# Kernel tuning notes

Measured on AMD Instinct MI355X. Metric: run time of the kernel, lower is better.

Reference implementation:

```python
import math
import jax, jax.numpy as jnp
import numpy as np

D_MODEL = 1024
NUM_HEADS = 16
MAX_SEQ_LEN = 2048
THETA = 10000.0


def setup_inputs() -> dict:
    key = jax.random.key(0)
    ks = jax.random.split(key, 5)
    B, S, D = 2, 2048, D_MODEL
    std = math.sqrt(2.0 / (D + D))
    x = jax.random.normal(ks[0], (B, S, D), dtype=jnp.float32)
    wq = jax.random.normal(ks[1], (D, D), dtype=jnp.float32) * std
    wk = jax.random.normal(ks[2], (D, D), dtype=jnp.float32) * std
    wv = jax.random.normal(ks[3], (D, D), dtype=jnp.float32) * std
    wo = jax.random.normal(ks[4], (D, D), dtype=jnp.float32) * std
    return {"x": x, "wq": wq, "wk": wk, "wv": wv, "wo": wo}


def _rope_tables(seq_len: int, d_k: int):
    # angles[i, k] = i / theta^(2k/d_k), k over d_k//2 pairs
    inv_freq = 1.0 / (THETA ** (jnp.arange(0, d_k, 2, dtype=jnp.float32) / d_k))
    angles = jnp.arange(seq_len, dtype=jnp.float32)[:, None] * inv_freq[None, :]  # [S, d_k/2]
    return jnp.cos(angles), jnp.sin(angles)


def _apply_rope(x, cos, sin):
    # x: [..., S, d_k]; cos/sin: [S, d_k/2], broadcast over leading dims
    x_even = x[..., ::2]
    x_odd = x[..., 1::2]
    r_even = x_even * cos - x_odd * sin
    r_odd = x_even * sin + x_odd * cos
    return jnp.stack([r_even, r_odd], axis=-1).reshape(x.shape)


def reference(x, wq, wk, wv, wo):
    B, S, D = x.shape
    H = NUM_HEADS
    dk = D // H

    def split_heads(t):  # [B,S,D] -> [B,H,S,dk]
        return t.reshape(B, S, H, dk).transpose(0, 2, 1, 3)

    Q = split_heads(x @ wq.T)
    K = split_heads(x @ wk.T)
    V = split_heads(x @ wv.T)

    cos, sin = _rope_tables(S, dk)
    Q = _apply_rope(Q, cos, sin)
    K = _apply_rope(K, cos, sin)

    scores = jnp.einsum('bhqd,bhkd->bhqk', Q, K) / jnp.sqrt(jnp.float32(dk))
    mask = jnp.tril(jnp.ones((S, S), dtype=bool))  # causal: q can attend k <= q
    neg_inf = jnp.float32(-jnp.inf)
    scores = jnp.where(mask, scores, neg_inf)
    m = jnp.max(scores, axis=-1, keepdims=True)
    m = jnp.where(jnp.isinf(m), jnp.zeros_like(m), m)
    exp_scores = jnp.exp(scores - m)
    exp_scores = jnp.where(mask, exp_scores, 0.0)
    attn = exp_scores / (jnp.sum(exp_scores, axis=-1, keepdims=True) + 1e-9)
    out = jnp.einsum('bhqk,bhkd->bhqd', attn, V)  # [B,H,S,dk]
    out = out.transpose(0, 2, 1, 3).reshape(B, S, D)
    return out @ wo.T
```

## Files before the change

kernel.cpp:

```cpp
#include <hip/hip_runtime.h>
#include <stdint.h>

typedef unsigned short u16;
typedef unsigned int u32;
typedef __bf16 bf16x8 __attribute__((ext_vector_type(8)));
typedef float f32x4 __attribute__((ext_vector_type(4)));
typedef unsigned short u16x8 __attribute__((ext_vector_type(8)));

#define D_MODEL 1024
#define SEQ 2048
#define NH 16
#define DK 64
#define NROWS 4096

static __device__ __forceinline__ u16 f2bf(float f) {
  u32 u = __float_as_uint(f);
  u = (u + 0x7FFFu + ((u >> 16) & 1u)) >> 16;
  return (u16)u;
}
static __device__ __forceinline__ float bf2f(u16 h) {
  return __uint_as_float(((u32)h) << 16);
}
static __device__ __forceinline__ f32x4 mfma16(bf16x8 a, bf16x8 b, f32x4 c) {
  return __builtin_amdgcn_mfma_f32_16x16x32_bf16(a, b, c, 0, 0, 0);
}
static __device__ __forceinline__ void gload16(const void* g, void* l) {
  __builtin_amdgcn_global_load_lds(
      (const __attribute__((address_space(1))) void*)g,
      (__attribute__((address_space(3))) void*)l, 16, 0, 0);
}

__global__ __launch_bounds__(256) void k_cast(
    const float* __restrict__ x, const float* __restrict__ wq,
    const float* __restrict__ wk, const float* __restrict__ wv,
    const float* __restrict__ wo, u16* __restrict__ xb, u16* __restrict__ wqb,
    u16* __restrict__ wkb, u16* __restrict__ wvb, u16* __restrict__ wob) {
  size_t e = ((size_t)blockIdx.x * 256 + threadIdx.x) * 8;
  const float* s;
  u16* d;
  size_t off;
  if (e < (size_t)NROWS * D_MODEL) {
    s = x; d = xb; off = e;
  } else {
    size_t r = e - (size_t)NROWS * D_MODEL;
    unsigned wi = (unsigned)(r >> 20);
    off = r & 1048575u;
    s = wi == 0 ? wq : wi == 1 ? wk : wi == 2 ? wv : wo;
    d = wi == 0 ? wqb : wi == 1 ? wkb : wi == 2 ? wvb : wob;
  }
  float4 a = *(const float4*)(s + off);
  float4 b = *(const float4*)(s + off + 4);
  u16x8 o;
  o[0] = f2bf(a.x); o[1] = f2bf(a.y); o[2] = f2bf(a.z); o[3] = f2bf(a.w);
  o[4] = f2bf(b.x); o[5] = f2bf(b.y); o[6] = f2bf(b.z); o[7] = f2bf(b.w);
  *(u16x8*)(d + off) = o;
}

__global__ __launch_bounds__(256) void k_tab(float* __restrict__ ct, float* __restrict__ st) {
  int i = blockIdx.x * 256 + threadIdx.x;
  int s = i >> 5, p = i & 31;
  double ang = (double)s * pow(10000.0, -(double)p / 32.0);
  ct[i] = (float)cos(ang);
  st[i] = (float)sin(ang);
}

template <bool MULTI, bool OUTF32>
__global__ __launch_bounds__(256, 1) void k_gemm(
    const u16* __restrict__ A, const u16* __restrict__ B0,
    const u16* __restrict__ B1, const u16* __restrict__ B2,
    u16* __restrict__ Cb, float* __restrict__ Cf, int ldc) {
  constexpr int K = 1024;
  const int mb = blockIdx.x, nb = blockIdx.y;
  const int tid = threadIdx.x;
  const int lane = tid & 63, w = tid >> 6;
  const int lq = lane & 15, lg = lane >> 4;
  const int wm = w >> 1, wn = w & 1;
  __shared__ __align__(16) u16 As[128 * 32];
  __shared__ __align__(16) u16 Bs[128 * 32];

  const u16* Bp;
  if (MULTI) {
    int sel = nb >> 3;
    Bp = sel == 0 ? B0 : (sel == 1 ? B1 : B2);
  } else {
    Bp = B0;
  }
  int nloc = MULTI ? (nb & 7) * 128 : nb * 128;
  const char* Ab = (const char*)A + (size_t)mb * 128 * 2048;
  const char* Bb = (const char*)Bp + (size_t)nloc * 2048;

  const int srow = tid >> 2;
  const int scb = (tid & 3) * 16;

  f32x4 zero4 = {0.f, 0.f, 0.f, 0.f};
  f32x4 acc[4][4];
#pragma unroll
  for (int i = 0; i < 4; ++i)
#pragma unroll
    for (int j = 0; j < 4; ++j) acc[i][j] = zero4;

  for (int k0 = 0; k0 < K; k0 += 32) {
#pragma unroll
    for (int c = 0; c < 2; ++c) {
      int o = c * 4096 + tid * 16;
      const char* ga = Ab + (size_t)(c * 64 + srow) * 2048 + k0 * 2 + scb;
      const char* gb = Bb + (size_t)(c * 64 + srow) * 2048 + k0 * 2 + scb;
      gload16(ga, (char*)As + o);
      gload16(gb, (char*)Bs + o);
    }
    __syncthreads();
    bf16x8 af[4], bfr[4];
#pragma unroll
    for (int i = 0; i < 4; ++i) {
      af[i] = *(const bf16x8*)((const char*)As + (wm * 64 + i * 16 + lq) * 64 + lg * 16);
      bfr[i] = *(const bf16x8*)((const char*)Bs + (wn * 64 + i * 16 + lq) * 64 + lg * 16);
    }
#pragma unroll
    for (int i = 0; i < 4; ++i)
#pragma unroll
      for (int j = 0; j < 4; ++j) acc[i][j] = mfma16(af[i], bfr[j], acc[i][j]);
    __syncthreads();
  }

#pragma unroll
  for (int i = 0; i < 4; ++i) {
#pragma unroll
    for (int r = 0; r < 4; ++r) {
      size_t rowg = (size_t)(mb * 128 + wm * 64 + i * 16 + lg * 4 + r);
#pragma unroll
      for (int j = 0; j < 4; ++j) {
        int colg = nb * 128 + wn * 64 + j * 16 + lq;
        if (OUTF32)
          Cf[rowg * ldc + colg] = acc[i][j][r];
        else
          Cb[rowg * ldc + colg] = f2bf(acc[i][j][r]);
      }
    }
  }
}

__global__ __launch_bounds__(256) void k_rope(const u16* __restrict__ qkv,
                                              const float* __restrict__ ct,
                                              const float* __restrict__ st,
                                              u16* __restrict__ qh, u16* __restrict__ kh) {
  int gi = blockIdx.x * 256 + threadIdx.x;
  int row = gi >> 7;
  int col = (gi & 127) << 3;
  int h = col >> 6, d0 = col & 63;
  int b = row >> 11, s = row & 2047;
  const int srcoff = blockIdx.y ? 1024 : 0;
  u16x8 v = *(const u16x8*)(qkv + (size_t)row * 3072 + srcoff + col);
  const float* cp = ct + s * 32 + (d0 >> 1);
  const float* sp = st + s * 32 + (d0 >> 1);
  u16x8 o;
#pragma unroll
  for (int i = 0; i < 4; ++i) {
    float ev = bf2f(v[2 * i]), od = bf2f(v[2 * i + 1]);
    float c = cp[i], sn = sp[i];
    o[2 * i] = f2bf(ev * c - od * sn);
    o[2 * i + 1] = f2bf(ev * sn + od * c);
  }
  u16* dst = blockIdx.y ? kh : qh;
  *(u16x8*)(dst + (((size_t)(b * 16 + h) * SEQ + s) << 6) + d0) = o;
}

__global__ __launch_bounds__(256) void k_vtrans(const u16* __restrict__ qkv,
                                                u16* __restrict__ vt) {
  __shared__ __align__(16) u16 t[64][72];
  int sb = blockIdx.x, bh = blockIdx.y;
  int b = bh >> 4, h = bh & 15;
  int tid = threadIdx.x;
#pragma unroll
  for (int c = 0; c < 2; ++c) {
    int o = tid * 8 + c * 2048;
    int r = o >> 6, d = o & 63;
    u16x8 v = *(const u16x8*)(qkv + (size_t)(b * SEQ + sb * 64 + r) * 3072 + 2048 + h * 64 + d);
    *(u16x8*)&t[r][d] = v;
  }
  __syncthreads();
#pragma unroll
  for (int c = 0; c < 2; ++c) {
    int o = tid * 8 + c * 2048;
    int d = o >> 6, si = o & 63;
    u16x8 v;
#pragma unroll
    for (int j = 0; j < 8; ++j) v[j] = t[si + j][d];
    *(u16x8*)(vt + ((size_t)bh * 64 + d) * SEQ + sb * 64 + si) = v;
  }
}

__global__ __launch_bounds__(512, 2) void k_attn(const u16* __restrict__ qh,
                                                 const u16* __restrict__ kh,
                                                 const u16* __restrict__ vt,
                                                 u16* __restrict__ ao) {
  const int xb_ = (int)blockIdx.x;
  const int qb = (xb_ & 1) ? (xb_ >> 1) : (15 - (xb_ >> 1));
  const int bh = blockIdx.y;
  const int tid = threadIdx.x;
  const int w = tid >> 6;
  const int lane = tid & 63;
  const int lq = lane & 15;
  const int lg = lane >> 4;

  __shared__ __align__(16) u16 Kl[64 * 64];
  __shared__ __align__(16) u16 Vl[64 * 64];
  __shared__ __align__(16) u16 Pl[8][16 * 64];

  const int q0 = qb * 128;
  const int qtop = q0 + w * 16;
  const int qrow = qtop + lq;

  const u16* qptr = qh + ((size_t)bh * SEQ + qrow) * DK + lg * 8;
  bf16x8 qf0 = *(const bf16x8*)qptr;
  bf16x8 qf1 = *(const bf16x8*)(qptr + 32);

  f32x4 zero4 = {0.f, 0.f, 0.f, 0.f};
  f32x4 accO[4];
  accO[0] = zero4; accO[1] = zero4; accO[2] = zero4; accO[3] = zero4;
  float m_run = -1e30f, l_run = 0.f;
  const float SCL = 0.180336880f;

  const int nkv = (qb + 1) * 2;
  const int srow = tid >> 3;
  const int scb = (tid & 7) * 16;

  uint4 kreg, vreg;
  kreg = *(const uint4*)((const char*)(kh + ((size_t)bh * SEQ + srow) * DK) + scb);
  vreg = *(const uint4*)((const char*)(vt + ((size_t)bh * DK + srow) * SEQ) + scb);

  for (int t = 0; t < nkv; ++t) {
    {
      int ad = (srow * 128 + scb) ^ ((srow & 7) << 4);
      *(uint4*)((char*)Kl + ad) = kreg;
      *(uint4*)((char*)Vl + ad) = vreg;
    }
    __syncthreads();

    uint4 k2, v2;
    if (t + 1 < nkv) {
      int k0n = (t + 1) * 64;
      k2 = *(const uint4*)((const char*)(kh + ((size_t)bh * SEQ + k0n + srow) * DK) + scb);
      v2 = *(const uint4*)((const char*)(vt + ((size_t)bh * DK + srow) * SEQ + k0n) + scb);
    } else {
      k2 = kreg; v2 = vreg;
    }

    const int k0 = t * 64;
    if (k0 <= qtop + 15) {
      f32x4 sa[4];
      sa[0] = zero4; sa[1] = zero4; sa[2] = zero4; sa[3] = zero4;
      __builtin_amdgcn_s_setprio(1);
#pragma unroll
      for (int kt = 0; kt < 4; ++kt) {
        int krow = kt * 16 + lq;
        int base = krow * 128 + lg * 16;
        int swz = (krow & 7) << 4;
        bf16x8 kf0 = *(const bf16x8*)((const char*)Kl + (base ^ swz));
        bf16x8 kf1 = *(const bf16x8*)((const char*)Kl + ((base + 64) ^ swz));
        sa[kt] = mfma16(kf0, qf0, sa[kt]);
        sa[kt] = mfma16(kf1, qf1, sa[kt]);
      }
      __builtin_amdgcn_s_setprio(0);

      float p[16];
      float pm = -1e30f;
#pragma unroll
      for (int kt = 0; kt < 4; ++kt) {
#pragma unroll
        for (int r = 0; r < 4; ++r) {
          int key = k0 + kt * 16 + lg * 4 + r;
          float sv = sa[kt][r] * SCL;
          sv = (key <= qrow) ? sv : -1e30f;
          p[kt * 4 + r] = sv;
          pm = fmaxf(pm, sv);
        }
      }
      pm = fmaxf(pm, __shfl_xor(pm, 16));
      pm = fmaxf(pm, __shfl_xor(pm, 32));
      const bool resc = __any(pm > m_run + 8.0f);
      float mnew = resc ? fmaxf(m_run, pm) : m_run;
      float rs = 0.f;
#pragma unroll
      for (int i = 0; i < 16; ++i) {
        p[i] = __builtin_amdgcn_exp2f(p[i] - mnew);
        rs += p[i];
      }
      rs += __shfl_xor(rs, 16);
      rs += __shfl_xor(rs, 32);
      if (resc) {
        float alpha = __builtin_amdgcn_exp2f(m_run - mnew);
        l_run = l_run * alpha + rs;
        m_run = mnew;
#pragma unroll
        for (int r = 0; r < 4; ++r) {
          float ar = __shfl(alpha, lg * 4 + r);
#pragma unroll
          for (int dt = 0; dt < 4; ++dt) accO[dt][r] *= ar;
        }
      } else {
        l_run += rs;
      }

      {
        int swz = (lq & 7) << 4;
#pragma unroll
        for (int kt = 0; kt < 4; ++kt) {
          u32 w0, w1;
          asm("v_cvt_pk_bf16_f32 %0, %1, %2"
              : "=v"(w0) : "v"(p[kt * 4 + 0]), "v"(p[kt * 4 + 1]));
          asm("v_cvt_pk_bf16_f32 %0, %1, %2"
              : "=v"(w1) : "v"(p[kt * 4 + 2]), "v"(p[kt * 4 + 3]));
          int a0 = (lq * 128 + (kt * 16 + lg * 4) * 2) ^ swz;
          int a1 = (lq * 128 + (kt * 16 + lg * 4 + 2) * 2) ^ swz;
          *(u32*)((char*)Pl[w] + a0) = w0;
          *(u32*)((char*)Pl[w] + a1) = w1;
        }
      }
      {
        int swz = (lq & 7) << 4;
        bf16x8 pa0 = *(const bf16x8*)((const char*)Pl[w] + ((lq * 128 + lg * 16) ^ swz));
        bf16x8 pa1 = *(const bf16x8*)((const char*)Pl[w] + ((lq * 128 + 64 + lg * 16) ^ swz));
        __builtin_amdgcn_s_setprio(1);
#pragma unroll
        for (int dt = 0; dt < 4; ++dt) {
          int vrow = dt * 16 + lq;
          int vb = vrow * 128 + lg * 16;
          int vs = (vrow & 7) << 4;
          bf16x8 v0 = *(const bf16x8*)((const char*)Vl + (vb ^ vs));
          bf16x8 v1 = *(const bf16x8*)((const char*)Vl + ((vb + 64) ^ vs));
          accO[dt] = mfma16(pa0, v0, accO[dt]);
          accO[dt] = mfma16(pa1, v1, accO[dt]);
        }
        __builtin_amdgcn_s_setprio(0);
      }
    }
    __syncthreads();
    kreg = k2; vreg = v2;
  }

  const int b = bh >> 4, h = bh & 15;
#pragma unroll
  for (int r = 0; r < 4; ++r) {
    float lr = __shfl(l_run, lg * 4 + r);
    float inv = 1.f / (lr + 1e-9f);
    int qq = qtop + lg * 4 + r;
    u16* orow = ao + ((size_t)b * SEQ + qq) * D_MODEL + h * DK;
#pragma unroll
    for (int dt = 0; dt < 4; ++dt) orow[dt * 16 + lq] = f2bf(accO[dt][r] * inv);
  }
}

extern "C" void kernel_launch(void* const* d_in, const int* in_sizes, int n_in,
                              void* d_out, int out_size, void* d_ws, size_t ws_size,
                              hipStream_t stream) {
  const float* x = (const float*)d_in[0];
  const float* wq = (const float*)d_in[1];
  const float* wk = (const float*)d_in[2];
  const float* wv = (const float*)d_in[3];
  const float* wo = (const float*)d_in[4];
  float* out = (float*)d_out;
  char* ws = (char*)d_ws;

  u16* xb   = (u16*)(ws + 0);
  u16* wqb  = (u16*)(ws + 8388608);
  u16* wkb  = (u16*)(ws + 10485760);
  u16* wvb  = (u16*)(ws + 12582912);
  u16* wob  = (u16*)(ws + 14680064);
  u16* qkv  = (u16*)(ws + 16777216);
  u16* qhb  = (u16*)(ws + 41943040);
  u16* khb  = (u16*)(ws + 50331648);
  u16* vtb  = (u16*)(ws + 58720256);
  u16* aob  = (u16*)(ws + 67108864);
  float* ct = (float*)(ws + 75497472);
  float* st = (float*)(ws + 75759616);

  k_cast<<<4096, 256, 0, stream>>>(x, wq, wk, wv, wo, xb, wqb, wkb, wvb, wob);
  k_tab<<<256, 256, 0, stream>>>(ct, st);
  k_gemm<true, false><<<dim3(32, 24), 256, 0, stream>>>(xb, wqb, wkb, wvb, qkv, nullptr, 3072);
  k_rope<<<dim3(2048, 2), 256, 0, stream>>>(qkv, ct, st, qhb, khb);
  k_vtrans<<<dim3(32, 32), 256, 0, stream>>>(qkv, vtb);
  k_attn<<<dim3(16, 32), 512, 0, stream>>>(qhb, khb, vtb, aob);
  k_gemm<false, true><<<dim3(32, 8), 256, 0, stream>>>(aob, wob, nullptr, nullptr, nullptr, out, 1024);
}
```

Baseline: 140.6 us.

## Pair complementary causal query blocks per workgroup with double-buffered direct LDS loads

Each attention workgroup now processes two query blocks (qb and 15-qb) so every block does equal causal work, and both query tiles reuse each K/V tile staged in shared memory. K/V loads go straight to a double-buffered LDS area via an async-style global-to-LDS load, replacing register staging. The grid is halved, so fewer workgroups run concurrently, and LDS use grows with the second buffer.

```diff
diff --git a/kernel.cpp b/kernel.cpp
--- a/kernel.cpp
+++ b/kernel.cpp
@@ -189,12 +189,105 @@
   }
 }
 
+static __device__ __forceinline__ void attn_tile(
+    const u16* Kl, const u16* Vl, u16* Plw, int k0, int qrow, int lq, int lg,
+    bf16x8 qf0, bf16x8 qf1, float& m_run, float& l_run, f32x4* accO) {
+  f32x4 zero4 = {0.f, 0.f, 0.f, 0.f};
+  const float SCL = 0.180336880f;
+  f32x4 sa[4];
+  sa[0] = zero4; sa[1] = zero4; sa[2] = zero4; sa[3] = zero4;
+  __builtin_amdgcn_s_setprio(1);
+#pragma unroll
+  for (int kt = 0; kt < 4; ++kt) {
+    int krow = kt * 16 + lq;
+    int base = krow * 128 + lg * 16;
+    int swz = (krow & 7) << 4;
+    bf16x8 kf0 = *(const bf16x8*)((const char*)Kl + (base ^ swz));
+    bf16x8 kf1 = *(const bf16x8*)((const char*)Kl + ((base + 64) ^ swz));
+    sa[kt] = mfma16(kf0, qf0, sa[kt]);
+    sa[kt] = mfma16(kf1, qf1, sa[kt]);
+  }
+  __builtin_amdgcn_s_setprio(0);
+
+  float p[16];
+  float pm = -1e30f;
+#pragma unroll
+  for (int kt = 0; kt < 4; ++kt) {
+#pragma unroll
+    for (int r = 0; r < 4; ++r) {
+      int key = k0 + kt * 16 + lg * 4 + r;
+      float sv = sa[kt][r] * SCL;
+      sv = (key <= qrow) ? sv : -1e30f;
+      p[kt * 4 + r] = sv;
+      pm = fmaxf(pm, sv);
+    }
+  }
+  pm = fmaxf(pm, __shfl_xor(pm, 16));
+  pm = fmaxf(pm, __shfl_xor(pm, 32));
+  const bool resc = __any(pm > m_run + 8.0f);
+  float mnew = resc ? fmaxf(m_run, pm) : m_run;
+  float rs = 0.f;
+#pragma unroll
+  for (int i = 0; i < 16; ++i) {
+    p[i] = __builtin_amdgcn_exp2f(p[i] - mnew);
+    rs += p[i];
+  }
+  rs += __shfl_xor(rs, 16);
+  rs += __shfl_xor(rs, 32);
+  if (resc) {
+    float alpha = __builtin_amdgcn_exp2f(m_run - mnew);
+    l_run = l_run * alpha + rs;
+    m_run = mnew;
+#pragma unroll
+    for (int r = 0; r < 4; ++r) {
+      float ar = __shfl(alpha, lg * 4 + r);
+#pragma unroll
+      for (int dt = 0; dt < 4; ++dt) accO[dt][r] *= ar;
+    }
+  } else {
+    l_run += rs;
+  }
+
+  {
+    int swz = (lq & 7) << 4;
+#pragma unroll
+    for (int kt = 0; kt < 4; ++kt) {
+      u32 w0, w1;
+      asm("v_cvt_pk_bf16_f32 %0, %1, %2"
+          : "=v"(w0) : "v"(p[kt * 4 + 0]), "v"(p[kt * 4 + 1]));
+      asm("v_cvt_pk_bf16_f32 %0, %1, %2"
+          : "=v"(w1) : "v"(p[kt * 4 + 2]), "v"(p[kt * 4 + 3]));
+      int a0 = (lq * 128 + (kt * 16 + lg * 4) * 2) ^ swz;
+      int a1 = (lq * 128 + (kt * 16 + lg * 4 + 2) * 2) ^ swz;
+      *(u32*)((char*)Plw + a0) = w0;
+      *(u32*)((char*)Plw + a1) = w1;
+    }
+  }
+  {
+    int swz = (lq & 7) << 4;
+    bf16x8 pa0 = *(const bf16x8*)((const char*)Plw + ((lq * 128 + lg * 16) ^ swz));
+    bf16x8 pa1 = *(const bf16x8*)((const char*)Plw + ((lq * 128 + 64 + lg * 16) ^ swz));
+    __builtin_amdgcn_s_setprio(1);
+#pragma unroll
+    for (int dt = 0; dt < 4; ++dt) {
+      int vrow = dt * 16 + lq;
+      int vb = vrow * 128 + lg * 16;
+      int vs = (vrow & 7) << 4;
+      bf16x8 v0 = *(const bf16x8*)((const char*)Vl + (vb ^ vs));
+      bf16x8 v1 = *(const bf16x8*)((const char*)Vl + ((vb + 64) ^ vs));
+      accO[dt] = mfma16(pa0, v0, accO[dt]);
+      accO[dt] = mfma16(pa1, v1, accO[dt]);
+    }
+    __builtin_amdgcn_s_setprio(0);
+  }
+}
+
 __global__ __launch_bounds__(512, 2) void k_attn(const u16* __restrict__ qh,
                                                  const u16* __restrict__ kh,
                                                  const u16* __restrict__ vt,
                                                  u16* __restrict__ ao) {
-  const int xb_ = (int)blockIdx.x;
-  const int qb = (xb_ & 1) ? (xb_ >> 1) : (15 - (xb_ >> 1));
+  const int qb1 = (int)blockIdx.x;
+  const int qb2 = 15 - qb1;
   const int bh = blockIdx.y;
   const int tid = threadIdx.x;
   const int w = tid >> 6;
@@ -202,151 +295,74 @@
   const int lq = lane & 15;
   const int lg = lane >> 4;
 
-  __shared__ __align__(16) u16 Kl[64 * 64];
-  __shared__ __align__(16) u16 Vl[64 * 64];
+  __shared__ __align__(16) u16 Kd[2][64 * 64];
+  __shared__ __align__(16) u16 Vd[2][64 * 64];
   __shared__ __align__(16) u16 Pl[8][16 * 64];
 
-  const int q0 = qb * 128;
-  const int qtop = q0 + w * 16;
-  const int qrow = qtop + lq;
-
-  const u16* qptr = qh + ((size_t)bh * SEQ + qrow) * DK + lg * 8;
-  bf16x8 qf0 = *(const bf16x8*)qptr;
-  bf16x8 qf1 = *(const bf16x8*)(qptr + 32);
+  const int qtop1 = qb1 * 128 + w * 16;
+  const int qtop2 = qb2 * 128 + w * 16;
+  const int qrow1 = qtop1 + lq;
+  const int qrow2 = qtop2 + lq;
+
+  const u16* qp1 = qh + ((size_t)bh * SEQ + qrow1) * DK + lg * 8;
+  const u16* qp2 = qh + ((size_t)bh * SEQ + qrow2) * DK + lg * 8;
+  bf16x8 qa0 = *(const bf16x8*)qp1;
+  bf16x8 qa1 = *(const bf16x8*)(qp1 + 32);
+  bf16x8 qb0 = *(const bf16x8*)qp2;
+  bf16x8 qb1f = *(const bf16x8*)(qp2 + 32);
 
   f32x4 zero4 = {0.f, 0.f, 0.f, 0.f};
-  f32x4 accO[4];
-  accO[0] = zero4; accO[1] = zero4; accO[2] = zero4; accO[3] = zero4;
-  float m_run = -1e30f, l_run = 0.f;
-  const float SCL = 0.180336880f;
-
-  const int nkv = (qb + 1) * 2;
+  f32x4 acc1[4], acc2[4];
+#pragma unroll
+  for (int dt = 0; dt < 4; ++dt) { acc1[dt] = zero4; acc2[dt] = zero4; }
+  float m1 = -1e30f, l1 = 0.f, m2 = -1e30f, l2 = 0.f;
+
+  const int NT = 2 * qb2 + 2;
+  const int nt1 = 2 * qb1 + (w >> 2) + 1;
+  const int nt2 = 2 * qb2 + (w >> 2) + 1;
+
   const int srow = tid >> 3;
   const int scb = (tid & 7) * 16;
-
-  uint4 kreg, vreg;
-  kreg = *(const uint4*)((const char*)(kh + ((size_t)bh * SEQ + srow) * DK) + scb);
-  vreg = *(const uint4*)((const char*)(vt + ((size_t)bh * DK + srow) * SEQ) + scb);
-
-  for (int t = 0; t < nkv; ++t) {
-    {
-      int ad = (srow * 128 + scb) ^ ((srow & 7) << 4);
-      *(uint4*)((char*)Kl + ad) = kreg;
-      *(uint4*)((char*)Vl + ad) = vreg;
-    }
+  const int colb = scb ^ ((srow & 7) << 4);
+  const char* kbase = (const char*)(kh + ((size_t)bh * SEQ + srow) * DK) + colb;
+  const char* vbase = (const char*)(vt + ((size_t)bh * DK + srow) * SEQ) + colb;
+
+  gload16(kbase, (char*)Kd[0] + tid * 16);
+  gload16(vbase, (char*)Vd[0] + tid * 16);
+  __syncthreads();
+
+  for (int t = 0; t < NT; ++t) {
+    const int cur = t & 1;
+    if (t + 1 < NT) {
+      gload16(kbase + (size_t)(t + 1) * 8192, (char*)Kd[cur ^ 1] + tid * 16);
+      gload16(vbase + (size_t)(t + 1) * 128, (char*)Vd[cur ^ 1] + tid * 16);
+    }
+    const int k0 = t * 64;
+    if (t < nt1)
+      attn_tile(Kd[cur], Vd[cur], Pl[w], k0, qrow1, lq, lg, qa0, qa1, m1, l1, acc1);
+    if (t < nt2)
+      attn_tile(Kd[cur], Vd[cur], Pl[w], k0, qrow2, lq, lg, qb0, qb1f, m2, l2, acc2);
     __syncthreads();
-
-    uint4 k2, v2;
-    if (t + 1 < nkv) {
-      int k0n = (t + 1) * 64;
-      k2 = *(const uint4*)((const char*)(kh + ((size_t)bh * SEQ + k0n + srow) * DK) + scb);
-      v2 = *(const uint4*)((const char*)(vt + ((size_t)bh * DK + srow) * SEQ + k0n) + scb);
-    } else {
-      k2 = kreg; v2 = vreg;
-    }
-
-    const int k0 = t * 64;
-    if (k0 <= qtop + 15) {
-      f32x4 sa[4];
-      sa[0] = zero4; sa[1] = zero4; sa[2] = zero4; sa[3] = zero4;
-      __builtin_amdgcn_s_setprio(1);
-#pragma unroll
-      for (int kt = 0; kt < 4; ++kt) {
-        int krow = kt * 16 + lq;
-        int base = krow * 128 + lg * 16;
-        int swz = (krow & 7) << 4;
-        bf16x8 kf0 = *(const bf16x8*)((const char*)Kl + (base ^ swz));
-        bf16x8 kf1 = *(const bf16x8*)((const char*)Kl + ((base + 64) ^ swz));
-        sa[kt] = mfma16(kf0, qf0, sa[kt]);
-        sa[kt] = mfma16(kf1, qf1, sa[kt]);
-      }
-      __builtin_amdgcn_s_setprio(0);
-
-      float p[16];
-      float pm = -1e30f;
-#pragma unroll
-      for (int kt = 0; kt < 4; ++kt) {
-#pragma unroll
-        for (int r = 0; r < 4; ++r) {
-          int key = k0 + kt * 16 + lg * 4 + r;
-          float sv = sa[kt][r] * SCL;
-          sv = (key <= qrow) ? sv : -1e30f;
-          p[kt * 4 + r] = sv;
-          pm = fmaxf(pm, sv);
-        }
-      }
-      pm = fmaxf(pm, __shfl_xor(pm, 16));
-      pm = fmaxf(pm, __shfl_xor(pm, 32));
-      const bool resc = __any(pm > m_run + 8.0f);
-      float mnew = resc ? fmaxf(m_run, pm) : m_run;
-      float rs = 0.f;
-#pragma unroll
-      for (int i = 0; i < 16; ++i) {
-        p[i] = __builtin_amdgcn_exp2f(p[i] - mnew);
-        rs += p[i];
-      }
-      rs += __shfl_xor(rs, 16);
-      rs += __shfl_xor(rs, 32);
-      if (resc) {
-        float alpha = __builtin_amdgcn_exp2f(m_run - mnew);
-        l_run = l_run * alpha + rs;
-        m_run = mnew;
-#pragma unroll
-        for (int r = 0; r < 4; ++r) {
-          float ar = __shfl(alpha, lg * 4 + r);
-#pragma unroll
-          for (int dt = 0; dt < 4; ++dt) accO[dt][r] *= ar;
-        }
-      } else {
-        l_run += rs;
-      }
-
-      {
-        int swz = (lq & 7) << 4;
-#pragma unroll
-        for (int kt = 0; kt < 4; ++kt) {
-          u32 w0, w1;
-          asm("v_cvt_pk_bf16_f32 %0, %1, %2"
-              : "=v"(w0) : "v"(p[kt * 4 + 0]), "v"(p[kt * 4 + 1]));
-          asm("v_cvt_pk_bf16_f32 %0, %1, %2"
-              : "=v"(w1) : "v"(p[kt * 4 + 2]), "v"(p[kt * 4 + 3]));
-          int a0 = (lq * 128 + (kt * 16 + lg * 4) * 2) ^ swz;
-          int a1 = (lq * 128 + (kt * 16 + lg * 4 + 2) * 2) ^ swz;
-          *(u32*)((char*)Pl[w] + a0) = w0;
-          *(u32*)((char*)Pl[w] + a1) = w1;
-        }
-      }
-      {
-        int swz = (lq & 7) << 4;
-        bf16x8 pa0 = *(const bf16x8*)((const char*)Pl[w] + ((lq * 128 + lg * 16) ^ swz));
-        bf16x8 pa1 = *(const bf16x8*)((const char*)Pl[w] + ((lq * 128 + 64 + lg * 16) ^ swz));
-        __builtin_amdgcn_s_setprio(1);
-#pragma unroll
-        for (int dt = 0; dt < 4; ++dt) {
-          int vrow = dt * 16 + lq;
-          int vb = vrow * 128 + lg * 16;
-          int vs = (vrow & 7) << 4;
-          bf16x8 v0 = *(const bf16x8*)((const char*)Vl + (vb ^ vs));
-          bf16x8 v1 = *(const bf16x8*)((const char*)Vl + ((vb + 64) ^ vs));
-          accO[dt] = mfma16(pa0, v0, accO[dt]);
-          accO[dt] = mfma16(pa1, v1, accO[dt]);
-        }
-        __builtin_amdgcn_s_setprio(0);
-      }
-    }
-    __syncthreads();
-    kreg = k2; vreg = v2;
   }
 
   const int b = bh >> 4, h = bh & 15;
 #pragma unroll
   for (int r = 0; r < 4; ++r) {
-    float lr = __shfl(l_run, lg * 4 + r);
+    float lr = __shfl(l1, lg * 4 + r);
     float inv = 1.f / (lr + 1e-9f);
-    int qq = qtop + lg * 4 + r;
+    int qq = qtop1 + lg * 4 + r;
     u16* orow = ao + ((size_t)b * SEQ + qq) * D_MODEL + h * DK;
 #pragma unroll
-    for (int dt = 0; dt < 4; ++dt) orow[dt * 16 + lq] = f2bf(accO[dt][r] * inv);
+    for (int dt = 0; dt < 4; ++dt) orow[dt * 16 + lq] = f2bf(acc1[dt][r] * inv);
+  }
+#pragma unroll
+  for (int r = 0; r < 4; ++r) {
+    float lr = __shfl(l2, lg * 4 + r);
+    float inv = 1.f / (lr + 1e-9f);
+    int qq = qtop2 + lg * 4 + r;
+    u16* orow = ao + ((size_t)b * SEQ + qq) * D_MODEL + h * DK;
+#pragma unroll
+    for (int dt = 0; dt < 4; ++dt) orow[dt * 16 + lq] = f2bf(acc2[dt][r] * inv);
   }
 }
 
@@ -379,6 +395,6 @@
   k_gemm<true, false><<<dim3(32, 24), 256, 0, stream>>>(xb, wqb, wkb, wvb, qkv, nullptr, 3072);
   k_rope<<<dim3(2048, 2), 256, 0, stream>>>(qkv, ct, st, qhb, khb);
   k_vtrans<<<dim3(32, 32), 256, 0, stream>>>(qkv, vtb);
-  k_attn<<<dim3(16, 32), 512, 0, stream>>>(qhb, khb, vtb, aob);
+  k_attn<<<dim3(8, 32), 512, 0, stream>>>(qhb, khb, vtb, aob);
   k_gemm<false, true><<<dim3(32, 8), 256, 0, stream>>>(aob, wob, nullptr, nullptr, nullptr, out, 1024);
 }
```

Result: faster. 132.1 us (-6.0%).
